# Kernel tuning notes

Measured on AMD Instinct MI355X. Metric: run time of the kernel, lower is better.

Reference implementation:

```python
import math
import jax, jax.numpy as jnp
import numpy as np

NUM_SEQS = 16
Q_LEN = 128           # uniform query tokens per sequence (cu_q_lens is uniform)
KV_HEADS = 8
Q_PER_GROUP = 4
HEAD_SIZE = 128
PAGE_SIZE = 64
PAGES_PER_SEQ = 16
NUM_PAGES = NUM_SEQS * PAGES_PER_SEQ
TOTAL_Q = NUM_SEQS * Q_LEN


def setup_inputs() -> dict:
    key = jax.random.key(0)
    k1, k2, k3 = jax.random.split(key, 3)
    q = jax.random.normal(k1, (TOTAL_Q, KV_HEADS, Q_PER_GROUP, HEAD_SIZE), dtype=jnp.float32)
    # combined kv_head axis holds K heads [0:H) then V heads [H:2H)
    kv_pages = jax.random.normal(k2, (NUM_PAGES, PAGE_SIZE, 2 * KV_HEADS, HEAD_SIZE), dtype=jnp.float32)
    # each sequence's KV length; >= Q_LEN so all new query tokens are in-context
    kv_lens = jax.random.randint(k3, (NUM_SEQS,), Q_LEN, PAGES_PER_SEQ * PAGE_SIZE + 1, dtype=jnp.int32)
    # distinct pages per sequence
    page_indices = jnp.arange(NUM_PAGES, dtype=jnp.int32).reshape(NUM_SEQS, PAGES_PER_SEQ)
    cu_q_lens = (jnp.arange(NUM_SEQS + 1, dtype=jnp.int32) * Q_LEN)
    return {
        "q": q,
        "kv_pages": kv_pages,
        "kv_lens": kv_lens,
        "page_indices": page_indices,
        "cu_q_lens": cu_q_lens,
        "num_seqs": NUM_SEQS,
    }


def _ragged_paged_attention(q, kv_pages, kv_lens, page_indices, num_seqs):
    T, H, G, D = q.shape
    S = num_seqs
    Q = T // S  # uniform per-seq query length (matches cu_q_lens)
    sm_scale = 1.0 / math.sqrt(D)
    qs = q.reshape(S, Q, H, G, D) * sm_scale  # [s q h g d]
    # gather pages: [S, P, page_size, 2H, D] -> [S, K, 2H, D]
    kv = kv_pages[page_indices].reshape(S, -1, 2 * H, D)
    K = kv.shape[1]
    k = kv[:, :, :H, :]  # [s k h d]
    v = kv[:, :, H:, :]  # [s k h d]
    # absolute position of each query token: kv_len - q_len + i
    q_pos = kv_lens[:, None] - Q + jnp.arange(Q)[None, :]          # [S, Q]
    kv_pos = jnp.arange(K)[None, None, :]                           # [1, 1, K]
    mask = (kv_pos <= q_pos[:, :, None]) & (kv_pos < kv_lens[:, None, None])  # [S, Q, K]
    scores = jnp.einsum("sqhgd,skhd->shgqk", qs, k)
    m4 = mask[:, None, None]  # [S,1,1,Q,K]
    a = jnp.where(m4, scores, -1e10)
    row_max = jnp.max(a, axis=-1, keepdims=True)
    p = jnp.where(m4, jnp.exp(a - row_max), 0.0)
    denom = jnp.maximum(jnp.sum(p, axis=-1), 1e-10)  # [S,H,G,Q]
    o = jnp.einsum("shgqk,skhd->sqhgd", p, v)
    o = o / jnp.transpose(denom, (0, 3, 1, 2))[..., None]
    return o.reshape(T, H, G, D)


def reference(q, kv_pages, kv_lens, page_indices, cu_q_lens, num_seqs):
    del cu_q_lens  # uniform layout encoded via num_seqs and q.shape[0]
    return _ragged_paged_attention(q, kv_pages, kv_lens, page_indices, num_seqs)
```

## Files before the change

kernel.cpp:

```cpp
#include <hip/hip_runtime.h>

typedef _Float16 f16;
typedef __attribute__((ext_vector_type(8))) _Float16 f16x8;
typedef __attribute__((ext_vector_type(4))) float f32x4;
typedef __fp16 fp16x2 __attribute__((ext_vector_type(2)));

#define NSEQ 16
#define QL   128
#define NH   8
#define NG   4
#define DH   128
#define PGSZ 64
#define PPS  16
#define KT   32
#define QIB  32
#define NQT  (QL / QIB)
#define THR_DEFER 11.0f

__device__ __forceinline__ unsigned cvt_pk_u32(float a, float b) {
    union { fp16x2 h2; unsigned u; } r;
    r.h2 = __builtin_amdgcn_cvt_pkrtz(a, b);
    return r.u;
}

__device__ __forceinline__ void bar_lds() {
    asm volatile("s_waitcnt lgkmcnt(0)" ::: "memory");
    __builtin_amdgcn_s_barrier();
    asm volatile("" ::: "memory");
}

__device__ __forceinline__ float fexp2(float x) {
    return __builtin_amdgcn_exp2f(x);
}

__global__ __launch_bounds__(512, 2)
void rpa_fwd(const float* __restrict__ q,
             const float* __restrict__ kv_pages,
             const int* __restrict__ kv_lens,
             const int* __restrict__ page_indices,
             float* __restrict__ out)
{
    const int tid  = threadIdx.x;
    const int wave = tid >> 6;
    const int lane = tid & 63;
    const int c16  = lane & 15;
    const int g16  = lane >> 4;

    const int qt = blockIdx.x;
    const int h  = blockIdx.y;

    int lens[16];
    #pragma unroll
    for (int i = 0; i < 16; ++i) lens[i] = kv_lens[i];
    const int z    = blockIdx.z;
    const int zmap = (z < 8) ? z : (23 - z);
    int s = 0;
    #pragma unroll
    for (int cand = 0; cand < 16; ++cand) {
        int r = 0;
        #pragma unroll
        for (int o = 0; o < 16; ++o)
            r += (lens[o] > lens[cand]) || (lens[o] == lens[cand] && o < cand);
        if (r == zmap) s = cand;
    }

    const int kv_len = lens[s];
    const int kv_end = kv_len - QL + qt*QIB + QIB;
    const int ntile  = (kv_end + KT - 1) / KT;

    __shared__ f16 Klds [2][KT*DH];
    __shared__ f16 VTlds[2][DH*KT];

    const int krow = tid >> 4;
    const int kslt = tid & 15;
    const int vkp2 = tid & 15;
    const int vd0  = (tid >> 4) * 4;

    const int sPPS = s * PPS;
    const int koff = (krow*(2*NH) + h)*DH + kslt*8;
    const int voff = ((2*vkp2)*(2*NH) + NH + h)*DH + vd0;

    f16x8 qfrag[4];
    {
        const int qiA = qt*QIB + wave*4 + (c16 >> 2);
        const int gA  = c16 & 3;
        const float* qp = q + (((size_t)(s*QL + qiA)*NH + h)*NG + gA)*DH;
        const float sc = 0.08838834764831845f * 1.4426950408889634f;
        #pragma unroll
        for (int sl = 0; sl < 4; ++sl) {
            const float* pp = qp + sl*32 + g16*8;
            f32x4 a = *(const f32x4*)pp;
            f32x4 b = *(const f32x4*)(pp + 4);
            union { unsigned u[4]; f16x8 v; } u;
            u.u[0] = cvt_pk_u32(a[0]*sc, a[1]*sc);
            u.u[1] = cvt_pk_u32(a[2]*sc, a[3]*sc);
            u.u[2] = cvt_pk_u32(b[0]*sc, b[1]*sc);
            u.u[3] = cvt_pk_u32(b[2]*sc, b[3]*sc);
            qfrag[sl] = u.v;
        }
    }

    const int q_pos_lane  = kv_len - QL + qt*QIB + wave*4 + (c16 >> 2);
    const int qp_wave_min = kv_len - QL + qt*QIB + wave*4;

    f32x4 oacc[8];
    #pragma unroll
    for (int f = 0; f < 8; ++f) oacc[f] = f32x4{0.f, 0.f, 0.f, 0.f};
    float mrun = -1e30f;
    float lrun = 0.f;

    f32x4 ka, kb, va, vb;

#define LOAD_TILE(T) do {                                                                \
        const int pg_ = page_indices[sPPS + ((T) >> 1)];       \
        const float* base_ = kv_pages + ((size_t)(pg_*PGSZ + ((T)&1)*32))*(2*NH*DH);     \
        ka = *(const f32x4*)(base_ + koff);                                              \
        kb = *(const f32x4*)(base_ + koff + 4);                                          \
        va = *(const f32x4*)(base_ + voff);                                              \
        vb = *(const f32x4*)(base_ + voff + 2*NH*DH);                                    \
    } while (0)

#define WRITE_TILE(BUF) do {                                                             \
        union { unsigned u[4]; f16x8 v; } ku_;                                           \
        ku_.u[0] = cvt_pk_u32(ka[0], ka[1]);                                             \
        ku_.u[1] = cvt_pk_u32(ka[2], ka[3]);                                             \
        ku_.u[2] = cvt_pk_u32(kb[0], kb[1]);                                             \
        ku_.u[3] = cvt_pk_u32(kb[2], kb[3]);                                             \
        *(f16x8*)((char*)&Klds[BUF][0]                                                   \
            + krow*256 + ((kslt ^ (krow & 7)) << 4)) = ku_.v;                            \
        _Pragma("unroll")                                                                \
        for (int j_ = 0; j_ < 4; ++j_) {                                                 \
            *(unsigned*)((char*)&VTlds[BUF][0]                                           \
                + (vd0 + j_)*64 + ((((vkp2 >> 2) ^ j_) << 4) + ((vkp2 & 3) << 2)))       \
                = cvt_pk_u32(va[j_], vb[j_]);                                            \
        }                                                                                \
    } while (0)

    LOAD_TILE(0);
    int buf = 0;

    for (int t = 0; t < ntile; ++t) {
        const int kv0 = t * KT;

        WRITE_TILE(buf);
        if (t + 1 < ntile) LOAD_TILE(t + 1);
        bar_lds();

        f32x4 sacc[2];
        sacc[0] = f32x4{0.f,0.f,0.f,0.f};
        sacc[1] = f32x4{0.f,0.f,0.f,0.f};
        __builtin_amdgcn_s_setprio(1);
        #pragma unroll
        for (int ks = 0; ks < 2; ++ks) {
            #pragma unroll
            for (int sl = 0; sl < 4; ++sl) {
                f16x8 kf = *(const f16x8*)((const char*)&Klds[buf][0]
                            + (ks*16 + c16)*256
                            + ((((sl << 2) | g16) ^ (c16 & 7)) << 4));
                sacc[ks] = __builtin_amdgcn_mfma_f32_16x16x32_f16(kf, qfrag[sl], sacc[ks], 0, 0, 0);
            }
        }
        __builtin_amdgcn_s_setprio(0);

        if (kv0 + KT - 1 > qp_wave_min) {
            #pragma unroll
            for (int ks = 0; ks < 2; ++ks)
                #pragma unroll
                for (int r = 0; r < 4; ++r)
                    if (kv0 + ks*16 + g16*4 + r > q_pos_lane)
                        sacc[ks][r] = -1e30f;
        }

        float m8 = fmaxf(fmaxf(fmaxf(sacc[0][0], sacc[0][1]), fmaxf(sacc[0][2], sacc[0][3])),
                         fmaxf(fmaxf(sacc[1][0], sacc[1][1]), fmaxf(sacc[1][2], sacc[1][3])));
        m8 = fmaxf(m8, __shfl_xor(m8, 16));
        m8 = fmaxf(m8, __shfl_xor(m8, 32));

        if (__any(m8 > mrun + THR_DEFER)) {
            const float mn  = fmaxf(mrun, m8);
            const float fac = fexp2(mrun - mn);
            lrun *= fac;
            mrun = mn;
            #pragma unroll
            for (int r = 0; r < 4; ++r) {
                const float fr = __shfl(fac, g16*4 + r);
                #pragma unroll
                for (int f = 0; f < 8; ++f) oacc[f][r] *= fr;
            }
        }

        float p0 = fexp2(sacc[0][0] - mrun), p1 = fexp2(sacc[0][1] - mrun);
        float p2 = fexp2(sacc[0][2] - mrun), p3 = fexp2(sacc[0][3] - mrun);
        float p4 = fexp2(sacc[1][0] - mrun), p5 = fexp2(sacc[1][1] - mrun);
        float p6 = fexp2(sacc[1][2] - mrun), p7 = fexp2(sacc[1][3] - mrun);
        float sm = ((p0 + p1) + (p2 + p3)) + ((p4 + p5) + (p6 + p7));
        sm += __shfl_xor(sm, 16);
        sm += __shfl_xor(sm, 32);
        lrun += sm;

        const unsigned A0 = cvt_pk_u32(p0, p1), A1 = cvt_pk_u32(p2, p3);
        const unsigned B0 = cvt_pk_u32(p4, p5), B1 = cvt_pk_u32(p6, p7);
        const int src0 = c16 + ((lane & 16) << 1);
        const int src1 = src0 + 16;
        const int a0 = __shfl((int)A0, src0), a1 = __shfl((int)A1, src0);
        const int b0 = __shfl((int)B0, src0), b1 = __shfl((int)B1, src0);
        const int e0 = __shfl((int)A0, src1), e1 = __shfl((int)A1, src1);
        const int f0 = __shfl((int)B0, src1), f1 = __shfl((int)B1, src1);
        const bool lo = (g16 < 2);
        union { int u[4]; f16x8 v; } pu;
        pu.u[0] = lo ? a0 : b0;
        pu.u[1] = lo ? a1 : b1;
        pu.u[2] = lo ? e0 : f0;
        pu.u[3] = lo ? e1 : f1;
        const f16x8 pf = pu.v;

        __builtin_amdgcn_s_setprio(1);
        #pragma unroll
        for (int f = 0; f < 8; ++f) {
            f16x8 vf = *(const f16x8*)((const char*)&VTlds[buf][0]
                        + (f*16 + c16)*64 + ((g16 ^ (c16 & 3)) << 4));
            oacc[f] = __builtin_amdgcn_mfma_f32_16x16x32_f16(pf, vf, oacc[f], 0, 0, 0);
        }
        __builtin_amdgcn_s_setprio(0);
        buf ^= 1;
    }

    const float linv = 1.f / fmaxf(lrun, 1e-10f);
    #pragma unroll
    for (int r = 0; r < 4; ++r) {
        const float ir = __shfl(linv, g16*4 + r);
        const int qi = qt*QIB + wave*4 + g16;
        float* op = out + (((size_t)(s*QL + qi)*NH + h)*NG + r)*DH;
        #pragma unroll
        for (int f = 0; f < 8; ++f)
            op[f*16 + c16] = oacc[f][r] * ir;
    }
}

extern "C" void kernel_launch(void* const* d_in, const int* in_sizes, int n_in,
                              void* d_out, int out_size, void* d_ws, size_t ws_size,
                              hipStream_t stream) {
    (void)in_sizes; (void)n_in; (void)d_ws; (void)ws_size; (void)out_size;
    const float* q         = (const float*)d_in[0];
    const float* kv_pages  = (const float*)d_in[1];
    const int*   kv_lens   = (const int*)d_in[2];
    const int*   page_idx  = (const int*)d_in[3];
    float* out = (float*)d_out;

    dim3 grid(NQT, NH, NSEQ);
    rpa_fwd<<<grid, 512, 0, stream>>>(q, kv_pages, kv_lens, page_idx, out);
}
```

Before: 70.68 us.

## Software-pipeline QK MFMA one tile ahead with triple-buffered LDS

After: 81.34 us. +15.1%, slower.

```diff
diff --git a/kernel.cpp b/kernel.cpp
--- a/kernel.cpp
+++ b/kernel.cpp
@@ -68,8 +68,8 @@
     const int kv_end = kv_len - QL + qt*QIB + QIB;
     const int ntile  = (kv_end + KT - 1) / KT;
 
-    __shared__ f16 Klds [2][KT*DH];
-    __shared__ f16 VTlds[2][DH*KT];
+    __shared__ f16 Klds [3][KT*DH];
+    __shared__ f16 VTlds[3][DH*KT];
 
     const int krow = tid >> 4;
     const int kslt = tid & 15;
@@ -120,59 +120,69 @@
         vb = *(const f32x4*)(base_ + voff + 2*NH*DH);                                    \
     } while (0)
 
-#define WRITE_TILE(BUF) do {                                                             \
+#define WRITE_TILE(BI) do {                                                              \
         union { unsigned u[4]; f16x8 v; } ku_;                                           \
         ku_.u[0] = cvt_pk_u32(ka[0], ka[1]);                                             \
         ku_.u[1] = cvt_pk_u32(ka[2], ka[3]);                                             \
         ku_.u[2] = cvt_pk_u32(kb[0], kb[1]);                                             \
         ku_.u[3] = cvt_pk_u32(kb[2], kb[3]);                                             \
-        *(f16x8*)((char*)&Klds[BUF][0]                                                   \
+        *(f16x8*)((char*)&Klds[BI][0]                                                    \
             + krow*256 + ((kslt ^ (krow & 7)) << 4)) = ku_.v;                            \
         _Pragma("unroll")                                                                \
         for (int j_ = 0; j_ < 4; ++j_) {                                                 \
-            *(unsigned*)((char*)&VTlds[BUF][0]                                           \
+            *(unsigned*)((char*)&VTlds[BI][0]                                            \
                 + (vd0 + j_)*64 + ((((vkp2 >> 2) ^ j_) << 4) + ((vkp2 & 3) << 2)))       \
                 = cvt_pk_u32(va[j_], vb[j_]);                                            \
         }                                                                                \
     } while (0)
 
+#define QK_TILE(S0, S1, BI) do {                                                         \
+        __builtin_amdgcn_s_setprio(1);                                                   \
+        _Pragma("unroll")                                                                \
+        for (int sl_ = 0; sl_ < 4; ++sl_) {                                              \
+            f16x8 kf0_ = *(const f16x8*)((const char*)&Klds[BI][0]                       \
+                        + c16*256 + ((((sl_ << 2) | g16) ^ (c16 & 7)) << 4));            \
+            S0 = __builtin_amdgcn_mfma_f32_16x16x32_f16(kf0_, qfrag[sl_], S0, 0, 0, 0);  \
+            f16x8 kf1_ = *(const f16x8*)((const char*)&Klds[BI][0]                       \
+                        + (16 + c16)*256 + ((((sl_ << 2) | g16) ^ (c16 & 7)) << 4));     \
+            S1 = __builtin_amdgcn_mfma_f32_16x16x32_f16(kf1_, qfrag[sl_], S1, 0, 0, 0);  \
+        }                                                                                \
+        __builtin_amdgcn_s_setprio(0);                                                   \
+    } while (0)
+
+    int bc = 0, bn = 1, b2 = 2;
     LOAD_TILE(0);
-    int buf = 0;
+    WRITE_TILE(bc);
+    if (ntile > 1) LOAD_TILE(1);
+    bar_lds();
+    f32x4 snext0 = f32x4{0.f,0.f,0.f,0.f};
+    f32x4 snext1 = f32x4{0.f,0.f,0.f,0.f};
+    QK_TILE(snext0, snext1, bc);
 
     for (int t = 0; t < ntile; ++t) {
         const int kv0 = t * KT;
-
-        WRITE_TILE(buf);
-        if (t + 1 < ntile) LOAD_TILE(t + 1);
-        bar_lds();
-
-        f32x4 sacc[2];
-        sacc[0] = f32x4{0.f,0.f,0.f,0.f};
-        sacc[1] = f32x4{0.f,0.f,0.f,0.f};
-        __builtin_amdgcn_s_setprio(1);
-        #pragma unroll
-        for (int ks = 0; ks < 2; ++ks) {
-            #pragma unroll
-            for (int sl = 0; sl < 4; ++sl) {
-                f16x8 kf = *(const f16x8*)((const char*)&Klds[buf][0]
-                            + (ks*16 + c16)*256
-                            + ((((sl << 2) | g16) ^ (c16 & 7)) << 4));
-                sacc[ks] = __builtin_amdgcn_mfma_f32_16x16x32_f16(kf, qfrag[sl], sacc[ks], 0, 0, 0);
-            }
-        }
-        __builtin_amdgcn_s_setprio(0);
+        f32x4 scur0 = snext0;
+        f32x4 scur1 = snext1;
+
+        if (t + 1 < ntile) {
+            WRITE_TILE(bn);
+            if (t + 2 < ntile) LOAD_TILE(t + 2);
+            bar_lds();
+            snext0 = f32x4{0.f,0.f,0.f,0.f};
+            snext1 = f32x4{0.f,0.f,0.f,0.f};
+            QK_TILE(snext0, snext1, bn);
+        }
 
         if (kv0 + KT - 1 > qp_wave_min) {
             #pragma unroll
-            for (int ks = 0; ks < 2; ++ks)
-                #pragma unroll
-                for (int r = 0; r < 4; ++r)
-                    if (kv0 + ks*16 + g16*4 + r > q_pos_lane)
-                        sacc[ks][r] = -1e30f;
-        }
-
-        float m8 = fmaxf(fmaxf(fmaxf(sacc[0][0], sacc[0][1]), fmaxf(sacc[0][2], sacc[0][3])),
-                         fmaxf(fmaxf(sacc[1][0], sacc[1][1]), fmaxf(sacc[1][2], sacc[1][3])));
+            for (int r = 0; r < 4; ++r) {
+                if (kv0 + g16*4 + r > q_pos_lane)      scur0[r] = -1e30f;
+                if (kv0 + 16 + g16*4 + r > q_pos_lane) scur1[r] = -1e30f;
+            }
+        }
+
+        float m8 = fmaxf(fmaxf(fmaxf(scur0[0], scur0[1]), fmaxf(scur0[2], scur0[3])),
+                         fmaxf(fmaxf(scur1[0], scur1[1]), fmaxf(scur1[2], scur1[3])));
         m8 = fmaxf(m8, __shfl_xor(m8, 16));
         m8 = fmaxf(m8, __shfl_xor(m8, 32));
 
@@ -189,14 +199,11 @@
             }
         }
 
-        float p0 = fexp2(sacc[0][0] - mrun), p1 = fexp2(sacc[0][1] - mrun);
-        float p2 = fexp2(sacc[0][2] - mrun), p3 = fexp2(sacc[0][3] - mrun);
-        float p4 = fexp2(sacc[1][0] - mrun), p5 = fexp2(sacc[1][1] - mrun);
-        float p6 = fexp2(sacc[1][2] - mrun), p7 = fexp2(sacc[1][3] - mrun);
-        float sm = ((p0 + p1) + (p2 + p3)) + ((p4 + p5) + (p6 + p7));
-        sm += __shfl_xor(sm, 16);
-        sm += __shfl_xor(sm, 32);
-        lrun += sm;
+        float p0 = fexp2(scur0[0] - mrun), p1 = fexp2(scur0[1] - mrun);
+        float p2 = fexp2(scur0[2] - mrun), p3 = fexp2(scur0[3] - mrun);
+        float p4 = fexp2(scur1[0] - mrun), p5 = fexp2(scur1[1] - mrun);
+        float p6 = fexp2(scur1[2] - mrun), p7 = fexp2(scur1[3] - mrun);
+        lrun += ((p0 + p1) + (p2 + p3)) + ((p4 + p5) + (p6 + p7));
 
         const unsigned A0 = cvt_pk_u32(p0, p1), A1 = cvt_pk_u32(p2, p3);
         const unsigned B0 = cvt_pk_u32(p4, p5), B1 = cvt_pk_u32(p6, p7);
@@ -217,14 +224,17 @@
         __builtin_amdgcn_s_setprio(1);
         #pragma unroll
         for (int f = 0; f < 8; ++f) {
-            f16x8 vf = *(const f16x8*)((const char*)&VTlds[buf][0]
+            f16x8 vf = *(const f16x8*)((const char*)&VTlds[bc][0]
                         + (f*16 + c16)*64 + ((g16 ^ (c16 & 3)) << 4));
             oacc[f] = __builtin_amdgcn_mfma_f32_16x16x32_f16(pf, vf, oacc[f], 0, 0, 0);
         }
         __builtin_amdgcn_s_setprio(0);
-        buf ^= 1;
-    }
-
+
+        const int tmp = bc; bc = bn; bn = b2; b2 = tmp;
+    }
+
+    lrun += __shfl_xor(lrun, 16);
+    lrun += __shfl_xor(lrun, 32);
     const float linv = 1.f / fmaxf(lrun, 1e-10f);
     #pragma unroll
     for (int r = 0; r < 4; ++r) {
```
